# Kernel optimization log

Hardware: AMD Instinct MI355X
Metric: run time of the kernel (lower is better)

The kernel has to match this reference:

```python
import jax, jax.numpy as jnp
import numpy as np

HW = 65536      # height*width = 256*256
C = 200         # spectral channels
NSP = 1024      # superpixels
E = 524288      # pixel-graph edges
D = 128         # hidden dim (hard-coded in module)
NCLS = 16
BN_EPS = 1e-5
LRELU = 0.01    # LeakyReLU default slope


def _l2norm(x):
    # F.normalize(x, dim=1)
    n = jnp.linalg.norm(x, axis=1, keepdims=True)
    return x / jnp.maximum(n, 1e-12)


def _bn(x):
    # BatchNorm1d, training-mode batch stats, default affine (gamma=1, beta=0)
    m = x.mean(0)
    v = x.var(0)
    return (x - m) * jax.lax.rsqrt(v + BN_EPS)


def _leaky(x):
    return jnp.where(x >= 0, x, LRELU * x)


def _gcn_conv(x, src, dst, W, b, n):
    # PyG GCNConv: add self-loops, sym-normalized aggregation, then bias
    xw = x @ W                                   # [n, D]
    deg = jnp.zeros((n,), x.dtype).at[dst].add(1.0) + 1.0  # incl. self-loop
    dinv = jax.lax.rsqrt(deg)
    norm = dinv[src] * dinv[dst]                 # [E]
    agg = jax.ops.segment_sum(xw[src] * norm[:, None], dst, num_segments=n)
    return agg + xw / deg[:, None] + b           # self-loop norm = 1/deg


def setup_inputs() -> dict:
    key = jax.random.key(0)
    ks = jax.random.split(key, 16)
    x = jax.random.normal(ks[0], (HW, C), jnp.float32)
    # one-hot superpixel assignment (every superpixel non-empty)
    seg = jnp.arange(HW, dtype=jnp.int32) % NSP
    seg = jax.random.permutation(ks[1], seg)
    Q = jax.nn.one_hot(seg, NSP, dtype=jnp.float32)
    # sparse-ish symmetric superpixel adjacency, normalized as in GCNLayer.__init__
    B = (jax.random.uniform(ks[2], (NSP, NSP)) < 0.01).astype(jnp.float32)
    A = jnp.maximum(B, B.T) * (1.0 - jnp.eye(NSP, dtype=jnp.float32))
    Ah = A + jnp.eye(NSP, dtype=jnp.float32)
    dinv = jax.lax.rsqrt(Ah.sum(1))
    A_norm = dinv[:, None] * Ah * dinv[None, :]
    edge_index = jax.random.randint(ks[3], (2, E), 0, HW, dtype=jnp.int32)
    s = 0.05
    return {
        'x': x, 'Q': Q, 'A_norm': A_norm, 'edge_index': edge_index,
        'prelin_W': jax.random.normal(ks[4], (C, D), jnp.float32) * s,
        'prelin_b': jnp.zeros((D,), jnp.float32),
        'gcn1_W': jax.random.normal(ks[5], (D, D), jnp.float32) * s,
        'gcn1_b': jnp.zeros((D,), jnp.float32),
        'gcn2_W': jax.random.normal(ks[6], (D, D), jnp.float32) * s,
        'gcn2_b': jnp.zeros((D,), jnp.float32),
        'mpnn1_W': jax.random.normal(ks[7], (D, D), jnp.float32) * s,
        'mpnn1_b': jnp.zeros((D,), jnp.float32),
        'mpnn2_W': jax.random.normal(ks[8], (D, D), jnp.float32) * s,
        'mpnn2_b': jnp.zeros((D,), jnp.float32),
        'out_W': jax.random.normal(ks[9], (D, NCLS), jnp.float32) * s,
        'out_b': jnp.zeros((NCLS,), jnp.float32),
    }


def reference(x, Q, A_norm, edge_index, prelin_W, prelin_b,
              gcn1_W, gcn1_b, gcn2_W, gcn2_b,
              mpnn1_W, mpnn1_b, mpnn2_W, mpnn2_b, out_W, out_b):
    # prelin + BN on pixels
    h = _bn(x @ prelin_W + prelin_b)             # [HW, D]
    # superpixel pooling (column-normalized Q), dense matmul as in original
    norm_col_Q = Q / Q.sum(0, keepdims=True)     # [HW, NSP]
    sp = norm_col_Q.T @ h                        # [NSP, D]

    def gcn_layer(H, W, b):
        return _leaky(A_norm @ (_bn(_l2norm(H)) @ W + b))

    H1 = gcn_layer(gcn_layer(sp, gcn1_W, gcn1_b), gcn2_W, gcn2_b)
    gcn_result = Q @ H1                          # unpool to pixels [HW, D]

    src, dst = edge_index[0], edge_index[1]

    def mpnn_layer(H, W, b):
        return _leaky(_gcn_conv(_bn(_l2norm(H)), src, dst, W, b, HW))

    m = mpnn_layer(mpnn_layer(h, mpnn1_W, mpnn1_b), mpnn2_W, mpnn2_b)
    logits = (m + gcn_result) @ out_W + out_b    # [HW, NCLS]
    return jax.nn.softmax(logits, axis=-1)
```

## Files before the change

kernel.cpp:

```cpp
#include <hip/hip_runtime.h>

#define HW 65536
#define NSP 1024
#define NE 524288
#define NCLS 16
#define BN_EPS 1e-5f
#define LSLOPE 0.01f

typedef unsigned short u16;
typedef short s16x8 __attribute__((ext_vector_type(8)));
typedef u16 u16x8 __attribute__((ext_vector_type(8)));
typedef u16 u16x4 __attribute__((ext_vector_type(4)));
typedef float f32x4 __attribute__((ext_vector_type(4)));

__device__ inline u16 f2b(float x) {
  unsigned int u = __float_as_uint(x);
  unsigned int r = ((u >> 16) & 1u) + 0x7FFFu;
  return (u16)((u + r) >> 16);
}
__device__ inline float b2f(u16 u) { return __uint_as_float(((unsigned int)u) << 16); }

struct P {
  const float *x, *Q, *A_norm;
  const int *e_src, *e_dst;
  const float *preW, *preB;
  const float *g1W, *g1b, *g2W, *g2b;
  const float *m1W, *m1b, *m2W, *m2b;
  const float *oW, *ob;
  float *outp;
  float *bufA, *bufB;
  int *cntd, *cntinv;
  float *stats;
  float *spDp, *spHp;
  int *seg, *seginv, *offp, *cur;
  float *dinv;
  int2 *e2;
  int *bsum;
  float *spA;
  float *xn1, *xn2, *z1p, *z2p, *rsums;
  float *WppG1, *WppG2;
  u16 *WTm1, *WTm2, *WTpre;
  float *cvG1, *bpG1, *cvG2, *bpG2, *cvM1, *bpM1, *cvM2, *bpM2;
  float *invG1, *invG2, *invM1;
  u16 *xb, *xwB, *bufN;
};

#define S_A(p)  ((p).stats + 0*256)
#define S_G1(p) ((p).stats + 1*256)
#define S_G2(p) ((p).stats + 2*256)
#define S_M1(p) ((p).stats + 3*256)
#define S_M2(p) ((p).stats + 4*256)

#define NQB 4096
#define NDB (NE / 256)
#define CXB (HW * 56 / 256)
#define CWB 112
#define RSB 256

__global__ __launch_bounds__(256) void k_setup(P p) {
  int b = blockIdx.x, t = threadIdx.x;
  int wv = t >> 6, lane = t & 63;
  if (b < NQB) {
    #pragma unroll
    for (int rr = 0; rr < 4; ++rr) {
      int row = (b * 4 + wv) * 4 + rr;
      const float4* qrow = (const float4*)(p.Q + (size_t)row * NSP);
      for (int c = 0; c < 4; ++c) {
        float4 v = qrow[c * 64 + lane];
        int hit = (v.x > 0.5f) || (v.y > 0.5f) || (v.z > 0.5f) || (v.w > 0.5f);
        unsigned long long m = __ballot(hit);
        if (m) {
          int L = (int)__ffsll((unsigned long long)m) - 1;
          if (lane == L) {
            int comp = (v.x > 0.5f) ? 0 : (v.y > 0.5f) ? 1 : (v.z > 0.5f) ? 2 : 3;
            int s = c * 256 + lane * 4 + comp;
            p.seg[row] = s;
            int pos = atomicAdd(&p.cntinv[s], 1);
            p.seginv[s * 64 + pos] = row;
          }
          break;
        }
      }
    }
  } else if (b < NQB + NDB) {
    int e = (b - NQB) * 256 + t;
    if (e < NE) atomicAdd(&p.cntd[p.e_dst[e]], 1);
  } else if (b < NQB + NDB + CXB) {
    int g = (b - NQB - NDB) * 256 + t;
    int row = g / 56, qd = g - row * 56;
    int k0 = qd * 4;
    u16x4 o;
    if (k0 < 200) {
      float4 v = *(const float4*)&p.x[(size_t)row * 200 + k0];
      o[0] = f2b(v.x); o[1] = f2b(v.y); o[2] = f2b(v.z); o[3] = f2b(v.w);
    } else { o[0] = 0; o[1] = 0; o[2] = 0; o[3] = 0; }
    *(u16x4*)&p.xb[(size_t)row * 224 + k0] = o;
  } else if (b < NQB + NDB + CXB + CWB) {
    int g = (b - NQB - NDB - CXB) * 256 + t;
    if (g < 128 * 224) {
      int n = g / 224, k = g - n * 224;
      p.WTpre[g] = (k < 200) ? f2b(p.preW[(size_t)k * 128 + n]) : (u16)0;
    }
  } else {
    int row = (b - NQB - NDB - CXB - CWB) * 4 + wv;
    const float4* ar = (const float4*)(p.A_norm + (size_t)row * NSP);
    float s = 0.f;
    #pragma unroll
    for (int c = 0; c < 4; ++c) {
      float4 v = ar[c * 64 + lane];
      s += v.x + v.y + v.z + v.w;
    }
    #pragma unroll
    for (int o = 1; o < 64; o <<= 1) s += __shfl_xor(s, o);
    if (lane == 0) p.rsums[row] = s;
  }
}

__device__ void dev_scan_a(P& p, int b, char* smem) {
  int* s = (int*)smem;
  int t = threadIdx.x;
  int i = b * 256 + t;
  int v = p.cntd[i];
  s[t] = v; __syncthreads();
  for (int o = 1; o < 256; o <<= 1) {
    int x = (t >= o) ? s[t - o] : 0;
    __syncthreads();
    s[t] += x;
    __syncthreads();
  }
  p.offp[i] = s[t] - v;
  if (t == 255) p.bsum[b] = s[t];
}

__device__ void dev_scan_c2(P& p, int b, char* smem) {
  int* w4 = (int*)smem;
  int t = threadIdx.x;
  int v = (t < b) ? p.bsum[t] : 0;
  #pragma unroll
  for (int o = 1; o < 64; o <<= 1) v += __shfl_xor(v, o);
  if ((t & 63) == 0) w4[t >> 6] = v;
  __syncthreads();
  int base = w4[0] + w4[1] + w4[2] + w4[3];
  int i = b * 256 + t;
  int ov = p.offp[i] + base;
  p.offp[i] = ov;
  p.cur[i] = ov;
  p.dinv[i] = rsqrtf((float)p.cntd[i] + 1.0f);
  if (i == 0) p.offp[HW] = NE;
}

__device__ void dev_scatter(P& p, int b) {
  int e = b * 256 + threadIdx.x;
  if (e < NE) {
    int d = p.e_dst[e], s = p.e_src[e];
    float w = p.dinv[d] * p.dinv[s];
    int pos = atomicAdd(&p.cur[d], 1);
    p.e2[pos] = make_int2(s, __float_as_int(w));
  }
}

__device__ void dev_mgemm(const void* Ap, int a_bf16, int lda,
                          const u16* WT, int ldb, int K,
                          const float* bias, const float* cvec, const float* invn,
                          void* Cp, int c_bf16,
                          float* sums, float* sumsq, int bid, char* smem) {
  u16* As = (u16*)smem;
  u16* Bs = (u16*)(smem + 10240);
  float* lsum = (float*)(smem + 30720);
  float* lssq = lsum + 128;
  int t = threadIdx.x;
  if (sums && t < 128) { lsum[t] = 0.f; lssq[t] = 0.f; }
  int row0 = bid * 64;
  int ar = t >> 2, ak = (t & 3) * 8;
  u16x8 aReg; u16x8 bReg[2];

  auto loadRegs = [&](int k0) {
    if (a_bf16) {
      aReg = *(const u16x8*)((const u16*)Ap + (size_t)(row0 + ar) * lda + k0 + ak);
    } else {
      const float* ap = (const float*)Ap + (size_t)(row0 + ar) * lda + k0 + ak;
      float4 f0 = *(const float4*)ap;
      float4 f1 = *(const float4*)(ap + 4);
      u16x8 v;
      v[0] = f2b(f0.x); v[1] = f2b(f0.y); v[2] = f2b(f0.z); v[3] = f2b(f0.w);
      v[4] = f2b(f1.x); v[5] = f2b(f1.y); v[6] = f2b(f1.z); v[7] = f2b(f1.w);
      aReg = v;
    }
    #pragma unroll
    for (int it = 0; it < 2; ++it) {
      int slot = t + it * 256;
      int bn = slot >> 2, kg = (slot & 3) * 8;
      bReg[it] = *(const u16x8*)(WT + (size_t)bn * ldb + k0 + kg);
    }
  };
  auto dsWrite = [&](int bq) {
    *(u16x8*)&As[(bq * 64 + ar) * 40 + ak] = aReg;
    #pragma unroll
    for (int it = 0; it < 2; ++it) {
      int slot = t + it * 256;
      int bn = slot >> 2, kg = (slot & 3) * 8;
      *(u16x8*)&Bs[(bq * 128 + bn) * 40 + kg] = bReg[it];
    }
  };

  int lane = t & 63, wvv = t >> 6;
  int m0 = (wvv >> 1) * 32, n0 = (wvv & 1) * 64;
  int fr = lane & 15, fk = (lane >> 4) * 8;
  f32x4 acc[2][4];
  #pragma unroll
  for (int mt = 0; mt < 2; ++mt)
    #pragma unroll
    for (int nt = 0; nt < 4; ++nt)
      acc[mt][nt] = (f32x4){0.f, 0.f, 0.f, 0.f};

  int nch = K >> 5;
  loadRegs(0);
  int cur = 0;
  for (int ch = 0; ch < nch; ++ch) {
    dsWrite(cur);
    __syncthreads();
    if (ch + 1 < nch) loadRegs((ch + 1) << 5);
    s16x8 afr0 = *(const s16x8*)&As[(cur * 64 + m0 + fr) * 40 + fk];
    s16x8 afr1 = *(const s16x8*)&As[(cur * 64 + m0 + 16 + fr) * 40 + fk];
    s16x8 bfr[4];
    #pragma unroll
    for (int nt = 0; nt < 4; ++nt)
      bfr[nt] = *(const s16x8*)&Bs[(cur * 128 + n0 + nt * 16 + fr) * 40 + fk];
    #pragma unroll
    for (int nt = 0; nt < 4; ++nt) {
      acc[0][nt] = __builtin_amdgcn_mfma_f32_16x16x32_bf16(afr0, bfr[nt], acc[0][nt], 0, 0, 0);
      acc[1][nt] = __builtin_amdgcn_mfma_f32_16x16x32_bf16(afr1, bfr[nt], acc[1][nt], 0, 0, 0);
    }
    cur ^= 1;
  }

  float bb4[4], cv4[4];
  #pragma unroll
  for (int nt = 0; nt < 4; ++nt) {
    int c = n0 + nt * 16 + fr;
    bb4[nt] = bias ? bias[c] : 0.f;
    cv4[nt] = cvec ? cvec[c] : 0.f;
  }
  int rg = lane >> 4;
  float cs4[4] = {}, cq4[4] = {};
  #pragma unroll
  for (int mt = 0; mt < 2; ++mt) {
    int rbase = row0 + m0 + mt * 16 + rg * 4;
    float inr[4];
    #pragma unroll
    for (int j = 0; j < 4; ++j) inr[j] = invn ? invn[rbase + j] : 1.f;
    #pragma unroll
    for (int nt = 0; nt < 4; ++nt) {
      int c = n0 + nt * 16 + fr;
      #pragma unroll
      for (int j = 0; j < 4; ++j) {
        float xv = inr[j] * (acc[mt][nt][j] - cv4[nt]) + bb4[nt];
        if (sums) { cs4[nt] += xv; cq4[nt] += xv * xv; }
        if (c_bf16) ((u16*)Cp)[(size_t)(rbase + j) * 128 + c] = f2b(xv);
        else        ((float*)Cp)[(size_t)(rbase + j) * 128 + c] = xv;
      }
    }
  }
  if (sums) {
    __syncthreads();
    #pragma unroll
    for (int nt = 0; nt < 4; ++nt) {
      int c = n0 + nt * 16 + fr;
      atomicAdd(&lsum[c], cs4[nt]);
      atomicAdd(&lssq[c], cq4[nt]);
    }
    __syncthreads();
    if (t < 128) { atomicAdd(&sums[t], lsum[t]); atomicAdd(&sumsq[t], lssq[t]); }
  }
}

__device__ void dev_pool2(P& p, int sp, char* smem) {
  float4* part = (float4*)smem;
  int t = threadIdx.x;
  int l32 = t & 31, g = t >> 5;
  int cnt = p.cntinv[sp];
  const float4* y4 = (const float4*)p.bufA;
  const int* lst = p.seginv + sp * 64;
  float4 acc = make_float4(0.f, 0.f, 0.f, 0.f);
  int r = g;
  for (; r + 8 < cnt; r += 16) {
    int i0 = lst[r], i1 = lst[r + 8];
    float4 a = y4[(size_t)i0 * 32 + l32];
    float4 b = y4[(size_t)i1 * 32 + l32];
    acc.x += a.x + b.x; acc.y += a.y + b.y;
    acc.z += a.z + b.z; acc.w += a.w + b.w;
  }
  for (; r < cnt; r += 8) {
    float4 a = y4[(size_t)lst[r] * 32 + l32];
    acc.x += a.x; acc.y += a.y; acc.z += a.z; acc.w += a.w;
  }
  part[g * 32 + l32] = acc;
  __syncthreads();
  if (g == 0) {
    float4 s = part[l32];
    #pragma unroll
    for (int q = 1; q < 8; ++q) {
      float4 pp = part[q * 32 + l32];
      s.x += pp.x; s.y += pp.y; s.z += pp.z; s.w += pp.w;
    }
    int d0 = l32 * 4;
    const float* sAs = S_A(p);
    const float* sAq = S_A(p) + 128;
    float4 ss = *(const float4*)&sAs[d0];
    float4 sq = *(const float4*)&sAq[d0];
    float inv = 1.0f / (float)cnt;
    float4 o;
    float m, rs;
    m = ss.x / HW; rs = rsqrtf(sq.x / HW - m * m + BN_EPS); o.x = (s.x * inv - m) * rs;
    m = ss.y / HW; rs = rsqrtf(sq.y / HW - m * m + BN_EPS); o.y = (s.y * inv - m) * rs;
    m = ss.z / HW; rs = rsqrtf(sq.z / HW - m * m + BN_EPS); o.z = (s.z * inv - m) * rs;
    m = ss.w / HW; rs = rsqrtf(sq.w / HW - m * m + BN_EPS); o.w = (s.w * inv - m) * rs;
    *(float4*)&p.spA[sp * 128 + d0] = o;
  }
}

__device__ void dev_rstats(const float* in, float* norm_out, float* invn,
                           float* sums, float* sumsq, int M,
                           const float* preS, const float* preQ, float precnt,
                           int leaky_in, int bid, int nb, char* smem) {
  float* lsum = (float*)smem;
  float* lssq = lsum + 128;
  int t = threadIdx.x;
  if (t < 128) { lsum[t] = 0.f; lssq[t] = 0.f; }
  __syncthreads();
  int wid = t >> 6, lane = t & 63, d0 = lane * 2;
  float m0 = 0.f, m1 = 0.f, r0 = 1.f, r1 = 1.f;
  if (preS) {
    m0 = preS[d0] / precnt;
    r0 = rsqrtf(preQ[d0] / precnt - m0 * m0 + BN_EPS);
    m1 = preS[d0 + 1] / precnt;
    r1 = rsqrtf(preQ[d0 + 1] / precnt - m1 * m1 + BN_EPS);
  }
  float cs0 = 0.f, cs1 = 0.f, cq0 = 0.f, cq1 = 0.f;
  for (int row = bid * 4 + wid; row < M; row += nb * 4) {
    float2 v = *(const float2*)(in + (size_t)row * 128 + d0);
    v.x = (v.x - m0) * r0;
    v.y = (v.y - m1) * r1;
    if (leaky_in) {
      v.x = (v.x >= 0.f) ? v.x : LSLOPE * v.x;
      v.y = (v.y >= 0.f) ? v.y : LSLOPE * v.y;
    }
    float ss = v.x * v.x + v.y * v.y;
    #pragma unroll
    for (int o = 1; o < 64; o <<= 1) ss += __shfl_xor(ss, o);
    float sc = 1.0f / fmaxf(sqrtf(ss), 1e-12f);
    if (lane == 0) invn[row] = sc;
    float nx = v.x * sc, ny = v.y * sc;
    if (norm_out) *(float2*)(norm_out + (size_t)row * 128 + d0) = make_float2(nx, ny);
    cs0 += nx; cs1 += ny; cq0 += nx * nx; cq1 += ny * ny;
  }
  atomicAdd(&lsum[d0], cs0); atomicAdd(&lsum[d0 + 1], cs1);
  atomicAdd(&lssq[d0], cq0); atomicAdd(&lssq[d0 + 1], cq1);
  __syncthreads();
  if (t < 128) { atomicAdd(&sums[t], lsum[t]); atomicAdd(&sumsq[t], lssq[t]); }
}

__device__ void dev_prepw(const float* sums, const float* sumsq, float cnt,
                          const float* W, const float* base,
                          const float* preS, const float* preQ, float precnt,
                          float* Wpp, u16* WT, float* cvec, float* bp, char* smem) {
  float* redc = (float*)smem;
  float* redb = redc + 1024;
  int t = threadIdx.x;
  int kq = (t & 31) * 4, jg = t >> 5;
  float cx = 0.f, cy = 0.f, cz = 0.f, cw = 0.f;
  float bx = 0.f, by = 0.f, bz = 0.f, bw = 0.f;
  for (int j = jg; j < 128; j += 8) {
    float m2 = sums[j] / cnt;
    float rs2 = rsqrtf(sumsq[j] / cnt - m2 * m2 + BN_EPS);
    float mA = 0.f, rsA = 1.f;
    if (preS) {
      mA = preS[j] / precnt;
      rsA = rsqrtf(preQ[j] / precnt - mA * mA + BN_EPS);
    }
    float4 w = *(const float4*)&W[j * 128 + kq];
    float sA = rsA * rs2;
    float4 wpp = make_float4(sA * w.x, sA * w.y, sA * w.z, sA * w.w);
    if (Wpp) *(float4*)&Wpp[j * 128 + kq] = wpp;
    if (WT) {
      WT[(size_t)(kq + 0) * 128 + j] = f2b(wpp.x);
      WT[(size_t)(kq + 1) * 128 + j] = f2b(wpp.y);
      WT[(size_t)(kq + 2) * 128 + j] = f2b(wpp.z);
      WT[(size_t)(kq + 3) * 128 + j] = f2b(wpp.w);
    }
    cx = fmaf(mA, wpp.x, cx); cy = fmaf(mA, wpp.y, cy);
    cz = fmaf(mA, wpp.z, cz); cw = fmaf(mA, wpp.w, cw);
    float m2s = m2 * rs2;
    bx = fmaf(m2s, w.x, bx); by = fmaf(m2s, w.y, by);
    bz = fmaf(m2s, w.z, bz); bw = fmaf(m2s, w.w, bw);
  }
  *(float4*)&redc[jg * 128 + kq] = make_float4(cx, cy, cz, cw);
  *(float4*)&redb[jg * 128 + kq] = make_float4(bx, by, bz, bw);
  __syncthreads();
  if (t < 32) {
    int k4 = t * 4;
    float4 sc = *(float4*)&redc[k4];
    float4 sb = *(float4*)&redb[k4];
    #pragma unroll
    for (int g = 1; g < 8; ++g) {
      float4 ac = *(float4*)&redc[g * 128 + k4];
      float4 ab = *(float4*)&redb[g * 128 + k4];
      sc.x += ac.x; sc.y += ac.y; sc.z += ac.z; sc.w += ac.w;
      sb.x += ab.x; sb.y += ab.y; sb.z += ab.z; sb.w += ab.w;
    }
    *(float4*)&cvec[k4] = sc;
    float4 bs = base ? *(const float4*)&base[k4] : make_float4(0, 0, 0, 0);
    *(float4*)&bp[k4] = make_float4(bs.x - sb.x, bs.y - sb.y, bs.z - sb.z, bs.w - sb.w);
  }
}

__device__ void dev_aggb(P& p, const u16* tbl, const float* bias, void* outp,
                         int norm_bf16, float* sums, float* sumsq,
                         int bid, int nb, char* smem) {
  float* lsum = (float*)smem;
  float* lssq = lsum + 128;
  int t = threadIdx.x;
  if (norm_bf16) {
    if (t < 128) { lsum[t] = 0.f; lssq[t] = 0.f; }
    __syncthreads();
  }
  int wid = t >> 6, lane = t & 63;
  int q = lane >> 4, l16 = lane & 15, c0 = l16 * 8;
  float bb[8];
  #pragma unroll
  for (int j = 0; j < 8; ++j) bb[j] = bias[c0 + j];
  float cs[8] = {}, cq[8] = {};
  for (int i = bid * 4 + wid; i < HW; i += nb * 4) {
    int s0 = p.offp[i], s1 = p.offp[i + 1];
    float di = p.dinv[i];
    u16x8 xi = *(const u16x8*)&tbl[(size_t)i * 128 + c0];
    float acc[8] = {};
    int kk = s0 + q;
    for (; kk + 4 < s1; kk += 8) {
      int2 ea = p.e2[kk], eb = p.e2[kk + 4];
      u16x8 va = *(const u16x8*)&tbl[(size_t)ea.x * 128 + c0];
      u16x8 vb = *(const u16x8*)&tbl[(size_t)eb.x * 128 + c0];
      float wa = __int_as_float(ea.y), wb = __int_as_float(eb.y);
      #pragma unroll
      for (int j = 0; j < 8; ++j) acc[j] = fmaf(wa, b2f(va[j]), acc[j]);
      #pragma unroll
      for (int j = 0; j < 8; ++j) acc[j] = fmaf(wb, b2f(vb[j]), acc[j]);
    }
    for (; kk < s1; kk += 4) {
      int2 e = p.e2[kk];
      u16x8 v = *(const u16x8*)&tbl[(size_t)e.x * 128 + c0];
      float w = __int_as_float(e.y);
      #pragma unroll
      for (int j = 0; j < 8; ++j) acc[j] = fmaf(w, b2f(v[j]), acc[j]);
    }
    #pragma unroll
    for (int j = 0; j < 8; ++j) {
      acc[j] += __shfl_xor(acc[j], 16);
      acc[j] += __shfl_xor(acc[j], 32);
    }
    float inv_deg = di * di;
    float r[8];
    #pragma unroll
    for (int j = 0; j < 8; ++j) {
      r[j] = fmaf(b2f(xi[j]), inv_deg, acc[j]) + bb[j];
      r[j] = (r[j] >= 0.f) ? r[j] : LSLOPE * r[j];
    }
    if (norm_bf16) {
      float ss = 0.f;
      #pragma unroll
      for (int j = 0; j < 8; ++j) ss += r[j] * r[j];
      ss += __shfl_xor(ss, 1); ss += __shfl_xor(ss, 2);
      ss += __shfl_xor(ss, 4); ss += __shfl_xor(ss, 8);
      float sc = 1.0f / fmaxf(sqrtf(ss), 1e-12f);
      if (q == 0) {
        u16x8 o;
        #pragma unroll
        for (int j = 0; j < 8; ++j) {
          r[j] *= sc;
          o[j] = f2b(r[j]);
          cs[j] += r[j]; cq[j] += r[j] * r[j];
        }
        *(u16x8*)&((u16*)outp)[(size_t)i * 128 + c0] = o;
      }
    } else if (q == 0) {
      float* op = (float*)outp + (size_t)i * 128 + c0;
      *(float4*)op = make_float4(r[0], r[1], r[2], r[3]);
      *(float4*)(op + 4) = make_float4(r[4], r[5], r[6], r[7]);
    }
  }
  if (norm_bf16) {
    if (q == 0) {
      #pragma unroll
      for (int j = 0; j < 8; ++j) {
        atomicAdd(&lsum[c0 + j], cs[j]);
        atomicAdd(&lssq[c0 + j], cq[j]);
      }
    }
    __syncthreads();
    if (t < 128) { atomicAdd(&sums[t], lsum[t]); atomicAdd(&sumsq[t], lssq[t]); }
  }
}

__device__ void dev_gemm_tail(const float* Z, const float* W,
                              const float* bp, const float* rs,
                              float* out, int bid) {
  int t = threadIdx.x;
  int c = t & 127, rh = t >> 7;
  int row0 = bid * 16 + rh * 8;
  float acc[8] = {};
  const float* ip = Z + (size_t)row0 * 128;
  #pragma unroll 4
  for (int k = 0; k < 128; ++k) {
    float w = W[k * 128 + c];
    #pragma unroll
    for (int i = 0; i < 8; ++i)
      acc[i] = fmaf(ip[(size_t)i * 128 + k], w, acc[i]);
  }
  float bpc = bp[c];
  #pragma unroll
  for (int i = 0; i < 8; ++i) {
    int row = row0 + i;
    out[(size_t)row * 128 + c] = acc[i] + rs[row] * bpc;
  }
}

__device__ void dev_gemm_ks(const float* A, const float* B, float* C,
                            int bid, char* smem) {
  float* As = (float*)smem;
  float* Bs = As + 32 * 68;
  int t = threadIdx.x;
  int c0 = (t & 31) * 4;
  int r0 = (t >> 5) * 8;
  int row0 = (bid >> 3) * 64;
  int kbeg = (bid & 7) * 128;
  int kend = kbeg + 128;
  int lr = t >> 2, lkb = (t & 3) * 8;
  float acc[8][4] = {};
  for (int k0 = kbeg; k0 < kend; k0 += 32) {
    __syncthreads();
    for (int idx = t * 4; idx < 32 * 128; idx += 1024)
      *(float4*)&Bs[(idx >> 7) * 128 + (idx & 127)] = *(const float4*)&B[(size_t)k0 * 128 + idx];
    {
      const float* ap = A + (size_t)(row0 + lr) * NSP + k0 + lkb;
      float4 v0 = *(const float4*)ap;
      float4 v1 = *(const float4*)(ap + 4);
      As[(lkb + 0) * 68 + lr] = v0.x; As[(lkb + 1) * 68 + lr] = v0.y;
      As[(lkb + 2) * 68 + lr] = v0.z; As[(lkb + 3) * 68 + lr] = v0.w;
      As[(lkb + 4) * 68 + lr] = v1.x; As[(lkb + 5) * 68 + lr] = v1.y;
      As[(lkb + 6) * 68 + lr] = v1.z; As[(lkb + 7) * 68 + lr] = v1.w;
    }
    __syncthreads();
    #pragma unroll 2
    for (int k = 0; k < 32; ++k) {
      float4 b4 = *(float4*)&Bs[k * 128 + c0];
      float4 a0 = *(float4*)&As[k * 68 + r0];
      float4 a1 = *(float4*)&As[k * 68 + r0 + 4];
      float av[8] = {a0.x, a0.y, a0.z, a0.w, a1.x, a1.y, a1.z, a1.w};
      float bv[4] = {b4.x, b4.y, b4.z, b4.w};
      #pragma unroll
      for (int r = 0; r < 8; ++r)
        #pragma unroll
        for (int c = 0; c < 4; ++c)
          acc[r][c] = fmaf(av[r], bv[c], acc[r][c]);
    }
  }
  #pragma unroll
  for (int r = 0; r < 8; ++r)
    #pragma unroll
    for (int c = 0; c < 4; ++c)
      atomicAdd(&C[(size_t)(row0 + r0 + r) * 128 + c0 + c], acc[r][c]);
}

__global__ __launch_bounds__(256) void k_za(P p) {
  __shared__ __align__(16) char smem[31744];
  int b = blockIdx.x;
  if (b < 256) dev_scan_a(p, b, smem);
  else dev_mgemm((const void*)p.xb, 1, 224, p.WTpre, 224, 224,
                 p.preB, nullptr, nullptr, (void*)p.bufA, 0,
                 S_A(p), S_A(p) + 128, b - 256, smem);
}
__global__ __launch_bounds__(256) void k_zb(P p) {
  __shared__ __align__(16) char smem[4096];
  int b = blockIdx.x;
  if (b < 256) dev_scan_c2(p, b, smem);
  else dev_pool2(p, b - 256, smem);
}
__global__ __launch_bounds__(256) void k_zc(P p) {
  __shared__ __align__(16) char smem[1024];
  int b = blockIdx.x;
  if (b < NE / 256) dev_scatter(p, b);
  else dev_rstats(p.bufA, nullptr, p.invM1, S_M1(p), S_M1(p) + 128, HW,
                  S_A(p), S_A(p) + 128, (float)HW, 0, b - NE / 256, 512, smem);
}
__global__ __launch_bounds__(256) void k_z8(P p) {
  __shared__ __align__(16) char smem[8192];
  int b = blockIdx.x;
  if (b < 16) dev_rstats(p.spA, p.xn1, p.invG1, S_G1(p), S_G1(p) + 128, NSP,
                         nullptr, nullptr, 1.f, 0, b, 16, smem);
  else dev_prepw(S_M1(p), S_M1(p) + 128, (float)HW, p.m1W, nullptr,
                 S_A(p), S_A(p) + 128, (float)HW,
                 nullptr, p.WTm1, p.cvM1, p.bpM1, smem);
}
__global__ __launch_bounds__(256) void k_z9(P p) {
  __shared__ __align__(16) char smem[31744];
  int b = blockIdx.x;
  if (b < 128) dev_gemm_ks(p.A_norm, p.xn1, p.z1p, b, smem);
  else if (b < 129) dev_prepw(S_G1(p), S_G1(p) + 128, (float)NSP, p.g1W, p.g1b,
                              nullptr, nullptr, 1.f, p.WppG1, nullptr, p.cvG1, p.bpG1, smem);
  else dev_mgemm((const void*)p.bufA, 0, 128, p.WTm1, 128, 128,
                 p.bpM1, p.cvM1, p.invM1, (void*)p.xwB, 1,
                 nullptr, nullptr, b - 129, smem);
}
__global__ __launch_bounds__(256) void k_z10(P p) {
  __shared__ __align__(16) char smem[1024];
  int b = blockIdx.x;
  if (b < 64) dev_gemm_tail(p.z1p, p.WppG1, p.bpG1, p.rsums, p.spDp, b);
  else dev_aggb(p, p.xwB, p.m1b, (void*)p.bufN, 1,
                S_M2(p), S_M2(p) + 128, b - 64, 2048, smem);
}
__global__ __launch_bounds__(256) void k_z11(P p) {
  __shared__ __align__(16) char smem[8192];
  int b = blockIdx.x;
  if (b < 1) dev_prepw(S_M2(p), S_M2(p) + 128, (float)HW, p.m2W, nullptr,
                       nullptr, nullptr, 1.f, nullptr, p.WTm2, p.cvM2, p.bpM2, smem);
  else dev_rstats(p.spDp, p.xn2, p.invG2, S_G2(p), S_G2(p) + 128, NSP,
                  nullptr, nullptr, 1.f, 1, b - 1, 16, smem);
}
__global__ __launch_bounds__(256) void k_z12(P p) {
  __shared__ __align__(16) char smem[31744];
  int b = blockIdx.x;
  if (b < 128) dev_gemm_ks(p.A_norm, p.xn2, p.z2p, b, smem);
  else if (b < 129) dev_prepw(S_G2(p), S_G2(p) + 128, (float)NSP, p.g2W, p.g2b,
                              nullptr, nullptr, 1.f, p.WppG2, nullptr, p.cvG2, p.bpG2, smem);
  else dev_mgemm((const void*)p.bufN, 1, 128, p.WTm2, 128, 128,
                 p.bpM2, p.cvM2, nullptr, (void*)p.xwB, 1,
                 nullptr, nullptr, b - 129, smem);
}
__global__ __launch_bounds__(256) void k_z13(P p) {
  __shared__ __align__(16) char smem[1024];
  int b = blockIdx.x;
  if (b < 64) dev_gemm_tail(p.z2p, p.WppG2, p.bpG2, p.rsums, p.spHp, b);
  else dev_aggb(p, p.xwB, p.m2b, (void*)p.bufB, 0,
                nullptr, nullptr, b - 64, 2048, smem);
}

__global__ __launch_bounds__(256) void k_final(P p) {
  __shared__ float rb[16][132];
  __shared__ float WL[128 * 16];
  int t = threadIdx.x;
  int row0 = blockIdx.x * 16;
  for (int idx = t; idx < 128 * NCLS; idx += 256) WL[idx] = p.oW[idx];
  for (int idx = t; idx < 16 * 128; idx += 256) {
    int r = idx >> 7, d = idx & 127;
    int row = row0 + r;
    float h = p.spHp[(size_t)p.seg[row] * 128 + d];
    h = (h >= 0.f) ? h : LSLOPE * h;
    rb[r][d] = p.bufB[(size_t)row * 128 + d] + h;
  }
  __syncthreads();
  int c = t & 15, r = t >> 4;
  float acc = p.ob[c];
  #pragma unroll 8
  for (int d = 0; d < 128; ++d) acc = fmaf(rb[r][d], WL[d * 16 + c], acc);
  float mx = acc;
  #pragma unroll
  for (int o = 1; o < 16; o <<= 1) mx = fmaxf(mx, __shfl_xor(mx, o));
  float e = expf(acc - mx);
  float s = e;
  #pragma unroll
  for (int o = 1; o < 16; o <<= 1) s += __shfl_xor(s, o);
  p.outp[(size_t)(row0 + r) * NCLS + c] = e / s;
}

extern "C" void kernel_launch(void* const* d_in, const int* in_sizes, int n_in,
                              void* d_out, int out_size, void* d_ws, size_t ws_size,
                              hipStream_t stream) {
  P p;
  p.x      = (const float*)d_in[0];
  p.Q      = (const float*)d_in[1];
  p.A_norm = (const float*)d_in[2];
  p.e_src  = (const int*)d_in[3];
  p.e_dst  = (const int*)d_in[3] + NE;
  p.preW = (const float*)d_in[4];  p.preB = (const float*)d_in[5];
  p.g1W  = (const float*)d_in[6];  p.g1b  = (const float*)d_in[7];
  p.g2W  = (const float*)d_in[8];  p.g2b  = (const float*)d_in[9];
  p.m1W  = (const float*)d_in[10]; p.m1b  = (const float*)d_in[11];
  p.m2W  = (const float*)d_in[12]; p.m2b  = (const float*)d_in[13];
  p.oW   = (const float*)d_in[14]; p.ob   = (const float*)d_in[15];
  p.outp = (float*)d_out;

  char* ws = (char*)d_ws;
  size_t o = 0;
  auto alloc = [&](size_t bytes) { size_t r = o; o = (o + bytes + 255) & ~255ULL; return r; };
  size_t bufA_o   = alloc((size_t)HW * 128 * 4);
  size_t bufB_o   = alloc((size_t)HW * 128 * 4);
  size_t cntd_o   = alloc((size_t)HW * 4);
  size_t cntinv_o = alloc((size_t)NSP * 4);
  size_t stats_o  = alloc(5 * 256 * 4);
  size_t z1p_o    = alloc((size_t)NSP * 128 * 4);
  size_t z2p_o    = alloc((size_t)NSP * 128 * 4);
  size_t zero_end = o;
  size_t spDp_o   = alloc((size_t)NSP * 128 * 4);
  size_t spHp_o   = alloc((size_t)NSP * 128 * 4);
  size_t seg_o    = alloc((size_t)HW * 4);
  size_t seginv_o = alloc((size_t)HW * 4);
  size_t off_o    = alloc((size_t)(HW + 1) * 4);
  size_t cur_o    = alloc((size_t)HW * 4);
  size_t dinv_o   = alloc((size_t)HW * 4);
  size_t e2_o     = alloc((size_t)NE * 8);
  size_t bsum_o   = alloc(256 * 4);
  size_t spA_o    = alloc((size_t)NSP * 128 * 4);
  size_t xn1_o    = alloc((size_t)NSP * 128 * 4);
  size_t xn2_o    = alloc((size_t)NSP * 128 * 4);
  size_t rsums_o  = alloc((size_t)NSP * 4);
  size_t WppG1_o  = alloc(128 * 128 * 4);
  size_t WppG2_o  = alloc(128 * 128 * 4);
  size_t WTm1_o   = alloc(128 * 128 * 2);
  size_t WTm2_o   = alloc(128 * 128 * 2);
  size_t WTpre_o  = alloc(128 * 224 * 2);
  size_t cvG1_o = alloc(512), bpG1_o = alloc(512);
  size_t cvG2_o = alloc(512), bpG2_o = alloc(512);
  size_t cvM1_o = alloc(512), bpM1_o = alloc(512);
  size_t cvM2_o = alloc(512), bpM2_o = alloc(512);
  size_t invG1_o  = alloc((size_t)NSP * 4);
  size_t invG2_o  = alloc((size_t)NSP * 4);
  size_t invM1_o  = alloc((size_t)HW * 4);
  size_t xb_o     = alloc((size_t)HW * 224 * 2);
  size_t xwB_o    = alloc((size_t)HW * 128 * 2);
  size_t bufN_o   = alloc((size_t)HW * 128 * 2);
  if (o > ws_size) return;

  p.bufA  = (float*)(ws + bufA_o);
  p.bufB  = (float*)(ws + bufB_o);
  p.cntd  = (int*)(ws + cntd_o);
  p.cntinv= (int*)(ws + cntinv_o);
  p.stats = (float*)(ws + stats_o);
  p.z1p   = (float*)(ws + z1p_o);
  p.z2p   = (float*)(ws + z2p_o);
  p.spDp  = (float*)(ws + spDp_o);
  p.spHp  = (float*)(ws + spHp_o);
  p.seg   = (int*)(ws + seg_o);
  p.seginv= (int*)(ws + seginv_o);
  p.offp  = (int*)(ws + off_o);
  p.cur   = (int*)(ws + cur_o);
  p.dinv  = (float*)(ws + dinv_o);
  p.e2    = (int2*)(ws + e2_o);
  p.bsum  = (int*)(ws + bsum_o);
  p.spA   = (float*)(ws + spA_o);
  p.xn1   = (float*)(ws + xn1_o);
  p.xn2   = (float*)(ws + xn2_o);
  p.rsums = (float*)(ws + rsums_o);
  p.WppG1 = (float*)(ws + WppG1_o);
  p.WppG2 = (float*)(ws + WppG2_o);
  p.WTm1  = (u16*)(ws + WTm1_o);
  p.WTm2  = (u16*)(ws + WTm2_o);
  p.WTpre = (u16*)(ws + WTpre_o);
  p.cvG1 = (float*)(ws + cvG1_o); p.bpG1 = (float*)(ws + bpG1_o);
  p.cvG2 = (float*)(ws + cvG2_o); p.bpG2 = (float*)(ws + bpG2_o);
  p.cvM1 = (float*)(ws + cvM1_o); p.bpM1 = (float*)(ws + bpM1_o);
  p.cvM2 = (float*)(ws + cvM2_o); p.bpM2 = (float*)(ws + bpM2_o);
  p.invG1 = (float*)(ws + invG1_o);
  p.invG2 = (float*)(ws + invG2_o);
  p.invM1 = (float*)(ws + invM1_o);
  p.xb   = (u16*)(ws + xb_o);
  p.xwB  = (u16*)(ws + xwB_o);
  p.bufN = (u16*)(ws + bufN_o);

  hipMemsetAsync(ws + cntd_o, 0, zero_end - cntd_o, stream);

  hipLaunchKernelGGL(k_setup, dim3(NQB + NDB + CXB + CWB + RSB), dim3(256), 0, stream, p);
  hipLaunchKernelGGL(k_za,    dim3(256 + HW / 64), dim3(256), 0, stream, p);
  hipLaunchKernelGGL(k_zb,    dim3(256 + NSP), dim3(256), 0, stream, p);
  hipLaunchKernelGGL(k_zc,    dim3(NE / 256 + 512), dim3(256), 0, stream, p);
  hipLaunchKernelGGL(k_z8,    dim3(17), dim3(256), 0, stream, p);
  hipLaunchKernelGGL(k_z9,    dim3(129 + HW / 64), dim3(256), 0, stream, p);
  hipLaunchKernelGGL(k_z10,   dim3(64 + 2048), dim3(256), 0, stream, p);
  hipLaunchKernelGGL(k_z11,   dim3(17), dim3(256), 0, stream, p);
  hipLaunchKernelGGL(k_z12,   dim3(129 + HW / 64), dim3(256), 0, stream, p);
  hipLaunchKernelGGL(k_z13,   dim3(64 + 2048), dim3(256), 0, stream, p);
  hipLaunchKernelGGL(k_final, dim3(HW / 16), dim3(256), 0, stream, p);
}
```

Baseline: 429.9 us.

## Split MPNN aggregation into column-slice gather plus separate normalization/stats pass

```diff
diff --git a/kernel.cpp b/kernel.cpp
--- a/kernel.cpp
+++ b/kernel.cpp
@@ -11,6 +11,7 @@
 typedef short s16x8 __attribute__((ext_vector_type(8)));
 typedef u16 u16x8 __attribute__((ext_vector_type(8)));
 typedef u16 u16x4 __attribute__((ext_vector_type(4)));
+typedef u16 u16x2 __attribute__((ext_vector_type(2)));
 typedef float f32x4 __attribute__((ext_vector_type(4)));
 
 __device__ inline u16 f2b(float x) {
@@ -38,6 +39,7 @@
   int *bsum;
   float *spA;
   float *xn1, *xn2, *z1p, *z2p, *rsums;
+  float *rowss, *invM2;
   float *WppG1, *WppG2;
   u16 *WTm1, *WTm2, *WTpre;
   float *cvG1, *bpG1, *cvG2, *bpG2, *cvM1, *bpM1, *cvM2, *bpM2;
@@ -414,91 +416,73 @@
   }
 }
 
-__device__ void dev_aggb(P& p, const u16* tbl, const float* bias, void* outp,
-                         int norm_bf16, float* sums, float* sumsq,
-                         int bid, int nb, char* smem) {
+__device__ void dev_agg_cs(P& p, const u16* tbl, const float* bias, void* outp,
+                           int mode, float* rowss, int bid) {
+  int t = threadIdx.x;
+  int wv = t >> 6, lane = t & 63;
+  int slot = lane >> 3, cl = lane & 7;
+  int g = bid & 7;
+  int c0 = g * 16 + cl * 2;
+  int rowbase = (bid >> 3) * 256 + wv * 64;
+  float b0 = bias[c0], b1 = bias[c0 + 1];
+  for (int r = 0; r < 64; ++r) {
+    int i = rowbase + r;
+    int s0 = p.offp[i], s1 = p.offp[i + 1];
+    float a0 = 0.f, a1 = 0.f;
+    for (int kk = s0; kk < s1; kk += 8) {
+      int idx = kk + slot;
+      if (idx < s1) {
+        int2 e = p.e2[idx];
+        float w = __int_as_float(e.y);
+        u16x2 v = *(const u16x2*)&tbl[(size_t)e.x * 128 + c0];
+        a0 = fmaf(w, b2f(v[0]), a0);
+        a1 = fmaf(w, b2f(v[1]), a1);
+      }
+    }
+    a0 += __shfl_xor(a0, 8);  a1 += __shfl_xor(a1, 8);
+    a0 += __shfl_xor(a0, 16); a1 += __shfl_xor(a1, 16);
+    a0 += __shfl_xor(a0, 32); a1 += __shfl_xor(a1, 32);
+    float di = p.dinv[i];
+    if (slot == 0) {
+      u16x2 xi = *(const u16x2*)&tbl[(size_t)i * 128 + c0];
+      float inv_deg = di * di;
+      float r0 = fmaf(b2f(xi[0]), inv_deg, a0) + b0;
+      float r1 = fmaf(b2f(xi[1]), inv_deg, a1) + b1;
+      r0 = (r0 >= 0.f) ? r0 : LSLOPE * r0;
+      r1 = (r1 >= 0.f) ? r1 : LSLOPE * r1;
+      if (mode) {
+        u16x2 o; o[0] = f2b(r0); o[1] = f2b(r1);
+        *(u16x2*)&((u16*)outp)[(size_t)i * 128 + c0] = o;
+        float pq = r0 * r0 + r1 * r1;
+        pq += __shfl_xor(pq, 1); pq += __shfl_xor(pq, 2); pq += __shfl_xor(pq, 4);
+        if (cl == 0) atomicAdd(&rowss[i], pq);
+      } else {
+        *(float2*)&((float*)outp)[(size_t)i * 128 + c0] = make_float2(r0, r1);
+      }
+    }
+  }
+}
+
+__device__ void dev_phaseB(P& p, int bid, int nb, char* smem) {
   float* lsum = (float*)smem;
   float* lssq = lsum + 128;
   int t = threadIdx.x;
-  if (norm_bf16) {
-    if (t < 128) { lsum[t] = 0.f; lssq[t] = 0.f; }
-    __syncthreads();
-  }
-  int wid = t >> 6, lane = t & 63;
-  int q = lane >> 4, l16 = lane & 15, c0 = l16 * 8;
-  float bb[8];
-  #pragma unroll
-  for (int j = 0; j < 8; ++j) bb[j] = bias[c0 + j];
-  float cs[8] = {}, cq[8] = {};
-  for (int i = bid * 4 + wid; i < HW; i += nb * 4) {
-    int s0 = p.offp[i], s1 = p.offp[i + 1];
-    float di = p.dinv[i];
-    u16x8 xi = *(const u16x8*)&tbl[(size_t)i * 128 + c0];
-    float acc[8] = {};
-    int kk = s0 + q;
-    for (; kk + 4 < s1; kk += 8) {
-      int2 ea = p.e2[kk], eb = p.e2[kk + 4];
-      u16x8 va = *(const u16x8*)&tbl[(size_t)ea.x * 128 + c0];
-      u16x8 vb = *(const u16x8*)&tbl[(size_t)eb.x * 128 + c0];
-      float wa = __int_as_float(ea.y), wb = __int_as_float(eb.y);
-      #pragma unroll
-      for (int j = 0; j < 8; ++j) acc[j] = fmaf(wa, b2f(va[j]), acc[j]);
-      #pragma unroll
-      for (int j = 0; j < 8; ++j) acc[j] = fmaf(wb, b2f(vb[j]), acc[j]);
-    }
-    for (; kk < s1; kk += 4) {
-      int2 e = p.e2[kk];
-      u16x8 v = *(const u16x8*)&tbl[(size_t)e.x * 128 + c0];
-      float w = __int_as_float(e.y);
-      #pragma unroll
-      for (int j = 0; j < 8; ++j) acc[j] = fmaf(w, b2f(v[j]), acc[j]);
-    }
-    #pragma unroll
-    for (int j = 0; j < 8; ++j) {
-      acc[j] += __shfl_xor(acc[j], 16);
-      acc[j] += __shfl_xor(acc[j], 32);
-    }
-    float inv_deg = di * di;
-    float r[8];
-    #pragma unroll
-    for (int j = 0; j < 8; ++j) {
-      r[j] = fmaf(b2f(xi[j]), inv_deg, acc[j]) + bb[j];
-      r[j] = (r[j] >= 0.f) ? r[j] : LSLOPE * r[j];
-    }
-    if (norm_bf16) {
-      float ss = 0.f;
-      #pragma unroll
-      for (int j = 0; j < 8; ++j) ss += r[j] * r[j];
-      ss += __shfl_xor(ss, 1); ss += __shfl_xor(ss, 2);
-      ss += __shfl_xor(ss, 4); ss += __shfl_xor(ss, 8);
-      float sc = 1.0f / fmaxf(sqrtf(ss), 1e-12f);
-      if (q == 0) {
-        u16x8 o;
-        #pragma unroll
-        for (int j = 0; j < 8; ++j) {
-          r[j] *= sc;
-          o[j] = f2b(r[j]);
-          cs[j] += r[j]; cq[j] += r[j] * r[j];
-        }
-        *(u16x8*)&((u16*)outp)[(size_t)i * 128 + c0] = o;
-      }
-    } else if (q == 0) {
-      float* op = (float*)outp + (size_t)i * 128 + c0;
-      *(float4*)op = make_float4(r[0], r[1], r[2], r[3]);
-      *(float4*)(op + 4) = make_float4(r[4], r[5], r[6], r[7]);
-    }
-  }
-  if (norm_bf16) {
-    if (q == 0) {
-      #pragma unroll
-      for (int j = 0; j < 8; ++j) {
-        atomicAdd(&lsum[c0 + j], cs[j]);
-        atomicAdd(&lssq[c0 + j], cq[j]);
-      }
-    }
-    __syncthreads();
-    if (t < 128) { atomicAdd(&sums[t], lsum[t]); atomicAdd(&sumsq[t], lssq[t]); }
-  }
+  if (t < 128) { lsum[t] = 0.f; lssq[t] = 0.f; }
+  __syncthreads();
+  int wid = t >> 6, lane = t & 63, d0 = lane * 2;
+  float cs0 = 0.f, cs1 = 0.f, cq0 = 0.f, cq1 = 0.f;
+  for (int row = bid * 4 + wid; row < HW; row += nb * 4) {
+    u16x2 v = *(const u16x2*)&p.bufN[(size_t)row * 128 + d0];
+    float ss = p.rowss[row];
+    float sc = 1.0f / fmaxf(sqrtf(ss), 1e-12f);
+    if (lane == 0) p.invM2[row] = sc;
+    float nx = b2f(v[0]) * sc, ny = b2f(v[1]) * sc;
+    cs0 += nx; cs1 += ny; cq0 += nx * nx; cq1 += ny * ny;
+  }
+  atomicAdd(&lsum[d0], cs0); atomicAdd(&lsum[d0 + 1], cs1);
+  atomicAdd(&lssq[d0], cq0); atomicAdd(&lssq[d0 + 1], cq1);
+  __syncthreads();
+  if (t < 128) { atomicAdd(&S_M2(p)[t], lsum[t]); atomicAdd(&(S_M2(p) + 128)[t], lssq[t]); }
 }
 
 __device__ void dev_gemm_tail(const float* Z, const float* W,
@@ -612,36 +596,37 @@
                  nullptr, nullptr, b - 129, smem);
 }
 __global__ __launch_bounds__(256) void k_z10(P p) {
+  int b = blockIdx.x;
+  if (b < 64) dev_gemm_tail(p.z1p, p.WppG1, p.bpG1, p.rsums, p.spDp, b);
+  else dev_agg_cs(p, p.xwB, p.m1b, (void*)p.bufN, 1, p.rowss, b - 64);
+}
+__global__ __launch_bounds__(256) void k_z10b(P p) {
   __shared__ __align__(16) char smem[1024];
   int b = blockIdx.x;
-  if (b < 64) dev_gemm_tail(p.z1p, p.WppG1, p.bpG1, p.rsums, p.spDp, b);
-  else dev_aggb(p, p.xwB, p.m1b, (void*)p.bufN, 1,
-                S_M2(p), S_M2(p) + 128, b - 64, 2048, smem);
+  if (b < 512) dev_phaseB(p, b, 512, smem);
+  else dev_rstats(p.spDp, p.xn2, p.invG2, S_G2(p), S_G2(p) + 128, NSP,
+                  nullptr, nullptr, 1.f, 1, b - 512, 16, smem);
 }
 __global__ __launch_bounds__(256) void k_z11(P p) {
   __shared__ __align__(16) char smem[8192];
   int b = blockIdx.x;
   if (b < 1) dev_prepw(S_M2(p), S_M2(p) + 128, (float)HW, p.m2W, nullptr,
                        nullptr, nullptr, 1.f, nullptr, p.WTm2, p.cvM2, p.bpM2, smem);
-  else dev_rstats(p.spDp, p.xn2, p.invG2, S_G2(p), S_G2(p) + 128, NSP,
-                  nullptr, nullptr, 1.f, 1, b - 1, 16, smem);
+  else dev_prepw(S_G2(p), S_G2(p) + 128, (float)NSP, p.g2W, p.g2b,
+                 nullptr, nullptr, 1.f, p.WppG2, nullptr, p.cvG2, p.bpG2, smem);
 }
 __global__ __launch_bounds__(256) void k_z12(P p) {
   __shared__ __align__(16) char smem[31744];
   int b = blockIdx.x;
   if (b < 128) dev_gemm_ks(p.A_norm, p.xn2, p.z2p, b, smem);
-  else if (b < 129) dev_prepw(S_G2(p), S_G2(p) + 128, (float)NSP, p.g2W, p.g2b,
-                              nullptr, nullptr, 1.f, p.WppG2, nullptr, p.cvG2, p.bpG2, smem);
   else dev_mgemm((const void*)p.bufN, 1, 128, p.WTm2, 128, 128,
-                 p.bpM2, p.cvM2, nullptr, (void*)p.xwB, 1,
-                 nullptr, nullptr, b - 129, smem);
+                 p.bpM2, p.cvM2, p.invM2, (void*)p.xwB, 1,
+                 nullptr, nullptr, b - 128, smem);
 }
 __global__ __launch_bounds__(256) void k_z13(P p) {
-  __shared__ __align__(16) char smem[1024];
   int b = blockIdx.x;
   if (b < 64) dev_gemm_tail(p.z2p, p.WppG2, p.bpG2, p.rsums, p.spHp, b);
-  else dev_aggb(p, p.xwB, p.m2b, (void*)p.bufB, 0,
-                nullptr, nullptr, b - 64, 2048, smem);
+  else dev_agg_cs(p, p.xwB, p.m2b, (void*)p.bufB, 0, nullptr, b - 64);
 }
 
 __global__ __launch_bounds__(256) void k_final(P p) {
@@ -699,6 +684,7 @@
   size_t stats_o  = alloc(5 * 256 * 4);
   size_t z1p_o    = alloc((size_t)NSP * 128 * 4);
   size_t z2p_o    = alloc((size_t)NSP * 128 * 4);
+  size_t rowss_o  = alloc((size_t)HW * 4);
   size_t zero_end = o;
   size_t spDp_o   = alloc((size_t)NSP * 128 * 4);
   size_t spHp_o   = alloc((size_t)NSP * 128 * 4);
@@ -713,6 +699,7 @@
   size_t xn1_o    = alloc((size_t)NSP * 128 * 4);
   size_t xn2_o    = alloc((size_t)NSP * 128 * 4);
   size_t rsums_o  = alloc((size_t)NSP * 4);
+  size_t invM2_o  = alloc((size_t)HW * 4);
   size_t WppG1_o  = alloc(128 * 128 * 4);
   size_t WppG2_o  = alloc(128 * 128 * 4);
   size_t WTm1_o   = alloc(128 * 128 * 2);
@@ -737,6 +724,7 @@
   p.stats = (float*)(ws + stats_o);
   p.z1p   = (float*)(ws + z1p_o);
   p.z2p   = (float*)(ws + z2p_o);
+  p.rowss = (float*)(ws + rowss_o);
   p.spDp  = (float*)(ws + spDp_o);
   p.spHp  = (float*)(ws + spHp_o);
   p.seg   = (int*)(ws + seg_o);
@@ -750,6 +738,7 @@
   p.xn1   = (float*)(ws + xn1_o);
   p.xn2   = (float*)(ws + xn2_o);
   p.rsums = (float*)(ws + rsums_o);
+  p.invM2 = (float*)(ws + invM2_o);
   p.WppG1 = (float*)(ws + WppG1_o);
   p.WppG2 = (float*)(ws + WppG2_o);
   p.WTm1  = (u16*)(ws + WTm1_o);
@@ -775,8 +764,9 @@
   hipLaunchKernelGGL(k_z8,    dim3(17), dim3(256), 0, stream, p);
   hipLaunchKernelGGL(k_z9,    dim3(129 + HW / 64), dim3(256), 0, stream, p);
   hipLaunchKernelGGL(k_z10,   dim3(64 + 2048), dim3(256), 0, stream, p);
-  hipLaunchKernelGGL(k_z11,   dim3(17), dim3(256), 0, stream, p);
-  hipLaunchKernelGGL(k_z12,   dim3(129 + HW / 64), dim3(256), 0, stream, p);
+  hipLaunchKernelGGL(k_z10b,  dim3(512 + 16), dim3(256), 0, stream, p);
+  hipLaunchKernelGGL(k_z11,   dim3(2), dim3(256), 0, stream, p);
+  hipLaunchKernelGGL(k_z12,   dim3(128 + HW / 64), dim3(256), 0, stream, p);
   hipLaunchKernelGGL(k_z13,   dim3(64 + 2048), dim3(256), 0, stream, p);
   hipLaunchKernelGGL(k_final, dim3(HW / 16), dim3(256), 0, stream, p);
 }
```

Result: slower. 793.8 us (+84.7%).
